# Performance work log

Measured on AMD Instinct MI355X. Metric: run time of the kernel, lower is better.

## Reference

```python
import jax, jax.numpy as jnp
import numpy as np

K = 3       # kernel_size
STRIDE = 1
PAD = 1

def _unfold(x, k, s, p):
    # torch.nn.functional.unfold with dilation=1; returns [N, C*k*k, L]
    N, C, H, W = x.shape
    out_H = (H - k + 2 * p) // s + 1
    out_W = (W - k + 2 * p) // s + 1
    xp = jnp.pad(x, ((0, 0), (0, 0), (p, p), (p, p)))
    # k*k = 9 static slices; ordering (c, kh, kw) matches torch unfold
    patches = [xp[:, :, i:i + (out_H - 1) * s + 1:s, j:j + (out_W - 1) * s + 1:s]
               for i in range(k) for j in range(k)]
    patches = jnp.stack(patches, axis=2)              # [N, C, k*k, out_H, out_W]
    return patches.reshape(N, C * k * k, out_H * out_W), out_H, out_W


def setup_inputs() -> dict:
    key = jax.random.key(0)
    k1, k2 = jax.random.split(key)
    N, C, H, W = 2, 32, 64, 64
    out_ch = 32
    L = H * W  # stride=1, pad=1, k=3 -> same spatial size
    features = jax.random.normal(k1, (N, C, H, W), dtype=jnp.float32)
    filters = jax.random.normal(k2, (N, L, C * K * K, out_ch), dtype=jnp.float32) * 0.05
    return {"features": features, "filters": filters}


def reference(features, filters):
    unf, out_H, out_W = _unfold(features, K, STRIDE, PAD)   # [N, Ckk, L]
    feat = unf.transpose(0, 2, 1)                           # [N, L, Ckk]
    # per-location matvec: [N,L,1,Ckk] @ [N,L,Ckk,O] -> [N,L,O]
    res = jnp.einsum('nlk,nlko->nol', feat, filters)        # [N, O, L]
    N = features.shape[0]
    res = res.reshape(N, filters.shape[-1], out_H, out_W)
    return jax.nn.relu(res)
```

## Files before the change

### kernel.cpp

```cpp
#include <hip/hip_runtime.h>


#define C_   32
#define H_   64
#define W_   64
#define O_   32
#define CKK_ 288
#define L_   (H_ * W_)

typedef float vf4 __attribute__((ext_vector_type(4)));

__global__ __launch_bounds__(256) void convfilt_kernel(
    const float* __restrict__ features,
    const float* __restrict__ filters,
    float* __restrict__ out)
{
    const int wave = threadIdx.x >> 6;
    const int lane = threadIdx.x & 63;
    const int loc  = blockIdx.x * 4 + wave;

    const int n  = loc >> 12;
    const int l  = loc & (L_ - 1);
    const int oh = l >> 6;
    const int ow = l & (W_ - 1);

    __shared__ float sf[4][CKK_];
    float* __restrict__ s = sf[wave];

    #pragma unroll
    for (int q = 0; q < 5; ++q) {
        const int e = q * 64 + lane;
        if (e < CKK_) {
            const int c  = e / 9;
            const int r  = e % 9;
            const int ih = oh + (r / 3) - 1;
            const int iw = ow + (r % 3) - 1;
            float v = 0.0f;
            if ((unsigned)ih < (unsigned)H_ && (unsigned)iw < (unsigned)W_)
                v = features[((n * C_ + c) * H_ + ih) * W_ + iw];
            s[e] = v;
        }
    }
    __syncthreads();

    const vf4* __restrict__ fp =
        (const vf4*)(filters + (size_t)loc * (CKK_ * O_));
    const int g = lane >> 3;

    float a0 = 0.f, a1 = 0.f, a2 = 0.f, a3 = 0.f;
    #pragma unroll
    for (int j = 0; j < 36; ++j) {
        const vf4  f  = __builtin_nontemporal_load(fp + j * 64 + lane);
        const float fv = s[j * 8 + g];
        a0 = fmaf(f.x, fv, a0);
        a1 = fmaf(f.y, fv, a1);
        a2 = fmaf(f.z, fv, a2);
        a3 = fmaf(f.w, fv, a3);
    }

    #pragma unroll
    for (int st = 8; st < 64; st <<= 1) {
        a0 += __shfl_down(a0, st);
        a1 += __shfl_down(a1, st);
        a2 += __shfl_down(a2, st);
        a3 += __shfl_down(a3, st);
    }

    if (lane < 8) {
        float* op = out + ((size_t)n * O_ + lane * 4) * L_ + l;
        op[0 * L_] = fmaxf(a0, 0.f);
        op[1 * L_] = fmaxf(a1, 0.f);
        op[2 * L_] = fmaxf(a2, 0.f);
        op[3 * L_] = fmaxf(a3, 0.f);
    }
}

extern "C" void kernel_launch(void* const* d_in, const int* in_sizes, int n_in,
                              void* d_out, int out_size, void* d_ws, size_t ws_size,
                              hipStream_t stream)
{
    const float* features = (const float*)d_in[0];
    const float* filters  = (const float*)d_in[1];
    float* out            = (float*)d_out;

    const int N     = in_sizes[0] / (C_ * H_ * W_);
    const int total = N * L_;
    const int grid  = total / 4;

    convfilt_kernel<<<grid, 256, 0, stream>>>(features, filters, out);
}
```

Measured before the change: 375.2 us.

## Split im2col into separate kernel and load patches as vectors

Adds a separate im2col kernel that writes the unfolded patches to workspace. The main kernel then loads each location's 288 patch values with coalesced vf4 loads instead of doing scattered gathers with divisions. It also swaps the nontemporal filter loads for regular loads and adds an occupancy hint to launch_bounds. The cost is an extra launch plus roughly 9.4 MB of patch writes and reads, on a kernel already bound by streaming about 75 MB of filters.

```diff
diff --git a/kernel.cpp b/kernel.cpp
--- a/kernel.cpp
+++ b/kernel.cpp
@@ -10,37 +10,49 @@
 
 typedef float vf4 __attribute__((ext_vector_type(4)));
 
-__global__ __launch_bounds__(256) void convfilt_kernel(
+__global__ __launch_bounds__(256) void im2col_kernel(
     const float* __restrict__ features,
+    float* __restrict__ patches,
+    int total)
+{
+    const int idx = blockIdx.x * 256 + threadIdx.x;
+    if (idx >= total) return;
+    const int loc = idx / CKK_;
+    const int k   = idx % CKK_;
+    const int n   = loc >> 12;
+    const int l   = loc & (L_ - 1);
+    const int oh  = l >> 6;
+    const int ow  = l & (W_ - 1);
+    const int c   = k / 9;
+    const int r   = k % 9;
+    const int ih  = oh + (r / 3) - 1;
+    const int iw  = ow + (r % 3) - 1;
+    float v = 0.0f;
+    if ((unsigned)ih < (unsigned)H_ && (unsigned)iw < (unsigned)W_)
+        v = features[((n * C_ + c) * H_ + ih) * W_ + iw];
+    patches[idx] = v;
+}
+
+__global__ __launch_bounds__(256, 4) void convfilt_kernel(
+    const float* __restrict__ patches,
     const float* __restrict__ filters,
     float* __restrict__ out)
 {
     const int wave = threadIdx.x >> 6;
     const int lane = threadIdx.x & 63;
     const int loc  = blockIdx.x * 4 + wave;
-
-    const int n  = loc >> 12;
-    const int l  = loc & (L_ - 1);
-    const int oh = l >> 6;
-    const int ow = l & (W_ - 1);
+    const int n    = loc >> 12;
+    const int l    = loc & (L_ - 1);
 
     __shared__ float sf[4][CKK_];
     float* __restrict__ s = sf[wave];
 
-    #pragma unroll
-    for (int q = 0; q < 5; ++q) {
-        const int e = q * 64 + lane;
-        if (e < CKK_) {
-            const int c  = e / 9;
-            const int r  = e % 9;
-            const int ih = oh + (r / 3) - 1;
-            const int iw = ow + (r % 3) - 1;
-            float v = 0.0f;
-            if ((unsigned)ih < (unsigned)H_ && (unsigned)iw < (unsigned)W_)
-                v = features[((n * C_ + c) * H_ + ih) * W_ + iw];
-            s[e] = v;
-        }
-    }
+    const vf4* __restrict__ pp = (const vf4*)(patches + (size_t)loc * CKK_);
+    vf4 pa = pp[lane];
+    vf4 pb;
+    if (lane < 8) pb = pp[64 + lane];
+    ((vf4*)s)[lane] = pa;
+    if (lane < 8) ((vf4*)s)[64 + lane] = pb;
     __syncthreads();
 
     const vf4* __restrict__ fp =
@@ -50,7 +62,7 @@
     float a0 = 0.f, a1 = 0.f, a2 = 0.f, a3 = 0.f;
     #pragma unroll
     for (int j = 0; j < 36; ++j) {
-        const vf4  f  = __builtin_nontemporal_load(fp + j * 64 + lane);
+        const vf4   f  = fp[j * 64 + lane];
         const float fv = s[j * 8 + g];
         a0 = fmaf(f.x, fv, a0);
         a1 = fmaf(f.y, fv, a1);
@@ -82,10 +94,12 @@
     const float* features = (const float*)d_in[0];
     const float* filters  = (const float*)d_in[1];
     float* out            = (float*)d_out;
+    float* patches        = (float*)d_ws;
 
     const int N     = in_sizes[0] / (C_ * H_ * W_);
-    const int total = N * L_;
-    const int grid  = total / 4;
+    const int nloc  = N * L_;
+    const int pelem = nloc * CKK_;
 
-    convfilt_kernel<<<grid, 256, 0, stream>>>(features, filters, out);
+    im2col_kernel<<<(pelem + 255) / 256, 256, 0, stream>>>(features, patches, pelem);
+    convfilt_kernel<<<nloc / 4, 256, 0, stream>>>(patches, filters, out);
 }
```

Result: slower. 409.4 us (+9.1%).
